# Kernel tuning notes

Measured on AMD Instinct MI355X. Metric: run time of the kernel, lower is better.

Reference implementation:

```python
import jax, jax.numpy as jnp
import numpy as np
from jax import lax

N_EXPERTS = 8
TOP_K_EXPERTS = 2
N_PRIMITIVES = 16
TOP_K_PRIM = 4
RANK = 64
D_MODEL = 512
D_FF = 2048
BATCH, SEQ = 8, 2048
TEMPERATURE = 1.0
EPS = 1e-8


def setup_inputs() -> dict:
    key = jax.random.key(0)
    ks = jax.random.split(key, 8)
    x = jax.random.normal(ks[0], (BATCH, SEQ, D_MODEL), dtype=jnp.float32)
    Wr = jax.random.normal(ks[1], (N_EXPERTS, D_MODEL), dtype=jnp.float32) * 0.02
    fc1_logits = jax.random.normal(ks[2], (N_EXPERTS, N_PRIMITIVES), dtype=jnp.float32)
    fc2_logits = jax.random.normal(ks[3], (N_EXPERTS, N_PRIMITIVES), dtype=jnp.float32)
    A1 = jax.random.normal(ks[4], (N_PRIMITIVES, D_MODEL, RANK), dtype=jnp.float32) * 0.02
    B1 = jax.random.normal(ks[5], (N_PRIMITIVES, RANK, D_FF), dtype=jnp.float32) * 0.02
    A2 = jax.random.normal(ks[6], (N_PRIMITIVES, D_FF, RANK), dtype=jnp.float32) * 0.02
    B2 = jax.random.normal(ks[7], (N_PRIMITIVES, RANK, D_MODEL), dtype=jnp.float32) * 0.02
    return {"x": x, "Wr": Wr, "fc1_logits": fc1_logits, "fc2_logits": fc2_logits,
            "A1": A1, "B1": B1, "A2": A2, "B2": B2}


def _compose_fused(logits, A, B):
    """Build per-expert fused low-rank maps from primitive bank.
    logits: (E, P); A: (P, d_in, r); B: (P, r, d_out).
    Returns A_cat (E, d_in, k*r), B_cat (E, k*r, d_out)."""
    w = jax.nn.softmax(logits / TEMPERATURE, axis=-1)            # (E, P)
    top_w, top_idx = lax.top_k(w, TOP_K_PRIM)                     # (E, k)
    top_w = top_w / (top_w.sum(axis=-1, keepdims=True) + EPS)
    sqrt_w = jnp.sqrt(top_w + EPS)                                # (E, k)
    A_sel = A[top_idx] * sqrt_w[:, :, None, None]                 # (E, k, d_in, r)
    B_sel = B[top_idx] * sqrt_w[:, :, None, None]                 # (E, k, r, d_out)
    E = logits.shape[0]
    A_cat = jnp.transpose(A_sel, (0, 2, 1, 3)).reshape(E, A.shape[1], TOP_K_PRIM * RANK)
    B_cat = B_sel.reshape(E, TOP_K_PRIM * RANK, B.shape[2])
    return A_cat, B_cat


def reference(x, Wr, fc1_logits, fc2_logits, A1, B1, A2, B2):
    Bsz, S, D = x.shape
    T = Bsz * S
    xt = x.reshape(T, D)

    # --- router: top-k expert selection ---
    router_logits = xt @ Wr.T                                     # (T, E)
    router_probs = jax.nn.softmax(router_logits, axis=-1)         # (T, E)
    top_w, top_idx = lax.top_k(router_probs, TOP_K_EXPERTS)       # (T, K)
    top_w = top_w / (top_w.sum(axis=-1, keepdims=True) + EPS)
    rows = jnp.arange(T)[:, None]
    gate = jnp.zeros((T, N_EXPERTS), x.dtype).at[rows, top_idx].add(top_w)
    expert_mask = jnp.zeros((T, N_EXPERTS), x.dtype).at[rows, top_idx].set(1.0)

    # --- load balancing aux loss (Switch Transformer) ---
    tokens_per_expert = expert_mask.sum(axis=0)
    f = tokens_per_expert / (tokens_per_expert.sum() + EPS)
    P = router_probs.mean(axis=0)
    aux_loss = N_EXPERTS * jnp.sum(f * P)

    # --- per-expert composed FFN over shared primitive banks ---
    A1c, B1c = _compose_fused(fc1_logits, A1, B1)                 # (E, D, kr), (E, kr, Dff)
    A2c, B2c = _compose_fused(fc2_logits, A2, B2)                 # (E, Dff, kr), (E, kr, D)

    out = jnp.zeros((T, D), x.dtype)
    for e in range(N_EXPERTS):  # small fixed expert loop keeps peak memory at one expert's d_ff activation
        h = jax.nn.gelu((xt @ A1c[e]) @ B1c[e], approximate=False)  # (T, Dff)
        y = (h @ A2c[e]) @ B2c[e]                                   # (T, D)
        out = out + gate[:, e:e + 1] * y

    return out.reshape(Bsz, S, D), aux_loss
```

## Files before the change

kernel.cpp:

```cpp
#include <hip/hip_runtime.h>

#define T_TOK 16384
#define DM    512
#define DFF   2048
#define NE    8
#define NP    16
#define KP    4
#define RANK  64
#define KR    256
#define EPSF  1e-8f
#define CAP   6144
#define MT_E  48

typedef unsigned short u16;
typedef __bf16 bf16x8 __attribute__((ext_vector_type(8)));
typedef float  f32x4  __attribute__((ext_vector_type(4)));
typedef unsigned short u16x8v __attribute__((ext_vector_type(8)));
typedef unsigned short u16x4v __attribute__((ext_vector_type(4)));

typedef __attribute__((address_space(3))) void as3_void;
typedef __attribute__((address_space(1))) void as1_void;

__device__ __forceinline__ u16 f2bf(float f) {
  return __builtin_bit_cast(u16, (__bf16)f);
}
__device__ __forceinline__ float bf2f(u16 v) {
  unsigned int u = ((unsigned int)v) << 16;
  return __builtin_bit_cast(float, u);
}

__device__ __forceinline__ void gl_lds16(const u16* g, u16* l) {
  __builtin_amdgcn_global_load_lds((as1_void*)g, (as3_void*)l, 16, 0, 0);
}


__device__ __forceinline__ void stage_tile(const u16* g, int ld, u16* lds_tile, int tid) {
  int row = tid >> 3, cc = tid & 7;
#pragma unroll
  for (int ri = 0; ri < 4; ri++) {
    int rg = ri * 32 + row;
    gl_lds16(g + (size_t)rg * ld + ((cc ^ (rg & 7)) * 8), &lds_tile[rg * 64 + cc * 8]);
  }
}

__device__ __forceinline__ void mfma_block(const u16* As, const u16* Bs, f32x4 acc[4][4],
                                           int wm, int wn, int ln, int quad) {
  int sw = (ln & 7) << 3;
#pragma unroll
  for (int ks = 0; ks < 2; ks++) {
    bf16x8 af[4], bf[4];
    int co = (ks * 32 + quad * 8) ^ sw;
#pragma unroll
    for (int mt = 0; mt < 4; mt++)
      af[mt] = *(const bf16x8*)&As[(wm * 64 + mt * 16 + ln) * 64 + co];
#pragma unroll
    for (int nt = 0; nt < 4; nt++)
      bf[nt] = *(const bf16x8*)&Bs[(wn * 64 + nt * 16 + ln) * 64 + co];
    __builtin_amdgcn_s_setprio(1);
#pragma unroll
    for (int mt = 0; mt < 4; mt++)
#pragma unroll
      for (int nt = 0; nt < 4; nt++)
        acc[mt][nt] = __builtin_amdgcn_mfma_f32_16x16x32_bf16(af[mt], bf[nt], acc[mt][nt], 0, 0, 0);
    __builtin_amdgcn_s_setprio(0);
  }
}

__global__ void zero_kernel(int* __restrict__ cnt, float* __restrict__ probsum) {
  int i = blockIdx.x * 256 + threadIdx.x;
  if (i < NE) cnt[i] = 0;
  if (i >= NE && i < NE + NE * 64) probsum[i - NE] = 0.f;
}

__global__ void compose_meta(const float* __restrict__ fc1, const float* __restrict__ fc2,
                             float* __restrict__ sw1, int* __restrict__ idx1,
                             float* __restrict__ sw2, int* __restrict__ idx2) {
  int tid = threadIdx.x;
  if (tid >= 16) return;
  const float* src = (tid < 8) ? fc1 : fc2;
  float* sw = (tid < 8) ? sw1 : sw2;
  int*  idx = (tid < 8) ? idx1 : idx2;
  int e = tid & 7;
  float wv[NP];
  float mx = -1e30f;
  for (int p = 0; p < NP; p++) { wv[p] = src[e * NP + p]; mx = fmaxf(mx, wv[p]); }
  float sum = 0.f;
  for (int p = 0; p < NP; p++) { wv[p] = __expf(wv[p] - mx); sum += wv[p]; }
  float inv = 1.f / sum;
  for (int p = 0; p < NP; p++) wv[p] *= inv;
  float tw[KP]; int ti[KP];
  for (int k = 0; k < KP; k++) {
    int best = 0; float bv = -1.f;
    for (int p = 0; p < NP; p++) if (wv[p] > bv) { bv = wv[p]; best = p; }
    tw[k] = bv; ti[k] = best; wv[best] = -2.f;
  }
  float ts = tw[0] + tw[1] + tw[2] + tw[3];
  float invt = 1.f / (ts + EPSF);
  for (int k = 0; k < KP; k++) {
    sw[e * KP + k] = sqrtf(tw[k] * invt + EPSF);
    idx[e * KP + k] = ti[k];
  }
}

__global__ __launch_bounds__(256) void build_AT(
    const float* __restrict__ A, const int* __restrict__ idx,
    const float* __restrict__ sw, u16* __restrict__ W, int D) {
  __shared__ u16 T[64 * 68];
  int ntile = D >> 6;
  int dt = blockIdx.x % ntile;
  int g  = blockIdx.x / ntile;
  int p = idx[g]; float s = sw[g];
  int d0 = dt * 64;
  int tid = threadIdx.x;
  {
    int rr = (tid & 15) * 4, dd = tid >> 4;
#pragma unroll
    for (int pass = 0; pass < 4; pass++) {
      int d = pass * 16 + dd;
      float4 v = *(const float4*)(A + ((size_t)p * D + d0 + d) * 64 + rr);
      T[(rr + 0) * 68 + d] = f2bf(v.x * s);
      T[(rr + 1) * 68 + d] = f2bf(v.y * s);
      T[(rr + 2) * 68 + d] = f2bf(v.z * s);
      T[(rr + 3) * 68 + d] = f2bf(v.w * s);
    }
  }
  __syncthreads();
  int e = g >> 2, k = g & 3;
  int c = (tid & 15) * 4, r = tid >> 4;
#pragma unroll
  for (int pass = 0; pass < 4; pass++) {
    int rr = pass * 16 + r;
    u16x4v o;
#pragma unroll
    for (int j = 0; j < 4; j++) o[j] = T[rr * 68 + c + j];
    *(u16x4v*)&W[((size_t)e * KR + k * 64 + rr) * D + d0 + c] = o;
  }
}

__global__ __launch_bounds__(256) void build_V1p(
    const float* __restrict__ B1, const int* __restrict__ idx1,
    const float* __restrict__ sw1, u16* __restrict__ V1p) {
  __shared__ u16 Tb[64 * 132];
  int bid = blockIdx.x;
  int p = bid & 3, f0i = (bid >> 2) & 15, e = bid >> 6;
  int prim = idx1[e * 4 + p];
  float s = sw1[e * 4 + p];
  int f0 = f0i * 128;
  int tid = threadIdx.x;
  {
    int r = tid >> 2, fq = (tid & 3) * 32;
#pragma unroll
    for (int q = 0; q < 8; q++) {
      int fl = fq + q * 4;
      float4 v = *(const float4*)(B1 + ((size_t)prim * RANK + r) * DFF + f0 + fl);
      u16x4v o;
      o[0] = f2bf(v.x * s); o[1] = f2bf(v.y * s);
      o[2] = f2bf(v.z * s); o[3] = f2bf(v.w * s);
      *(u16x4v*)&Tb[r * 132 + fl] = o;
    }
  }
  __syncthreads();
  u16* dst = V1p + ((size_t)e << 19) + f0i * 32768 + p * 8192;
#pragma unroll
  for (int it = 0; it < 4; it++) {
    int slot = it * 256 + tid;
    int lane = slot & 63, nt = (slot >> 6) & 1, ks = (slot >> 7) & 1, wv = slot >> 8;
    int ln = lane & 15, quad = lane >> 4;
    int fl = wv * 32 + nt * 16 + ln;
    int r0 = ks * 32 + quad * 8;
    u16x8v o;
#pragma unroll
    for (int j = 0; j < 8; j++) o[j] = Tb[(r0 + j) * 132 + fl];
    *(u16x8v*)&dst[(((wv * 2 + ks) * 2 + nt) * 64 + lane) * 8] = o;
  }
}

__global__ __launch_bounds__(256) void build_W2p(
    const float* __restrict__ A2, const int* __restrict__ idx2,
    const float* __restrict__ sw2, u16* __restrict__ W2p) {
  __shared__ u16 Ta[2 * 64 * 68];
  int bid = blockIdx.x;
  int c2 = bid & 3, f0i = (bid >> 2) & 15, e = bid >> 6;
  int hh = c2 >> 1, fi = c2 & 1;
  int f0 = f0i * 128 + fi * 64;
  int tid = threadIdx.x;
  {
    int kk = tid >> 7, row = (tid >> 1) & 63, half = tid & 1;
    int prim = idx2[e * 4 + hh * 2 + kk];
    float s = sw2[e * 4 + hh * 2 + kk];
#pragma unroll
    for (int q = 0; q < 8; q++) {
      int r = half * 32 + q * 4;
      float4 v = *(const float4*)(A2 + ((size_t)prim * DFF + f0 + row) * RANK + r);
      u16x4v o;
      o[0] = f2bf(v.x * s); o[1] = f2bf(v.y * s);
      o[2] = f2bf(v.z * s); o[3] = f2bf(v.w * s);
      *(u16x4v*)&Ta[(kk * 64 + row) * 68 + r] = o;
    }
  }
  __syncthreads();
  u16* dst = W2p + ((size_t)e << 19) + f0i * 32768 + c2 * 8192;
#pragma unroll
  for (int it = 0; it < 4; it++) {
    int slot = it * 256 + tid;
    int lane = slot & 63, nt = (slot >> 6) & 1, ks = (slot >> 7) & 1, wv = slot >> 8;
    int ln = lane & 15, quad = lane >> 4;
    int kk = wv >> 1;
    int r = (wv & 1) * 32 + nt * 16 + ln;
    int fb = ks * 32 + quad * 8;
    u16x8v o;
#pragma unroll
    for (int j = 0; j < 8; j++) o[j] = Ta[(kk * 64 + fb + j) * 68 + r];
    *(u16x8v*)&dst[(((wv * 2 + ks) * 2 + nt) * 64 + lane) * 8] = o;
  }
}

__global__ void build_V2(const float* __restrict__ B2,
                         const float* __restrict__ sw2, const int* __restrict__ idx2,
                         u16* __restrict__ V2) {
  const int S4 = NE * DM * KR;
  int j = blockIdx.x * 256 + threadIdx.x;
  if (j < S4) {
    int kr = j & 255; int d = (j >> 8) & 511; int e = j >> 17;
    int k = kr >> 6, r = kr & 63; int p = idx2[e * 4 + k];
    V2[j] = f2bf(B2[((size_t)p * RANK + r) * DM + d] * sw2[e * 4 + k]);
  }
}

__global__ __launch_bounds__(256) void router_kernel(
    const float* __restrict__ x, const float* __restrict__ Wr,
    float* __restrict__ probsum, int* __restrict__ eidx,
    float* __restrict__ gate) {
  __shared__ float wr_s[NE * 4 * 132];
  __shared__ float ps_s[NE];
  int tid = threadIdx.x;
  if (tid < NE) ps_s[tid] = 0.f;
  for (int i = tid; i < NE * DM; i += 256) {
    int e = i >> 9, k = i & 511;
    wr_s[(e * 4 + (k >> 7)) * 132 + (k & 127)] = Wr[i];
  }
  __syncthreads();
  int lane = tid & 63, wv = tid >> 6;
  int tl = lane & 15, sl = lane >> 4;
  int t = blockIdx.x * 64 + wv * 16 + tl;
  const float* xp = x + (size_t)t * DM + sl * 128;
  const float* wp = &wr_s[sl * 132];
  float acc[NE];
#pragma unroll
  for (int e = 0; e < NE; e++) acc[e] = 0.f;
  for (int c = 0; c < 32; c++) {
    float4 xv = *(const float4*)(xp + c * 4);
#pragma unroll
    for (int e = 0; e < NE; e++) {
      float4 w4 = *(const float4*)(wp + e * 4 * 132 + c * 4);
      acc[e] += xv.x * w4.x + xv.y * w4.y + xv.z * w4.z + xv.w * w4.w;
    }
  }
#pragma unroll
  for (int e = 0; e < NE; e++) {
    acc[e] += __shfl_xor(acc[e], 16, 64);
    acc[e] += __shfl_xor(acc[e], 32, 64);
  }
  if (sl == 0) {
    float mx = acc[0];
#pragma unroll
    for (int e = 1; e < NE; e++) mx = fmaxf(mx, acc[e]);
    float pe[NE]; float sum = 0.f;
#pragma unroll
    for (int e = 0; e < NE; e++) { pe[e] = __expf(acc[e] - mx); sum += pe[e]; }
    float inv = 1.f / sum;
#pragma unroll
    for (int e = 0; e < NE; e++) pe[e] *= inv;
    int i0 = 0;
#pragma unroll
    for (int e = 1; e < NE; e++) if (pe[e] > pe[i0]) i0 = e;
    int i1 = (i0 == 0) ? 1 : 0;
#pragma unroll
    for (int e = 0; e < NE; e++) if (e != i0 && pe[e] > pe[i1]) i1 = e;
    float p0 = pe[i0], p1 = pe[i1];
    float gd = 1.f / (p0 + p1 + EPSF);
    eidx[t] = i0 | (i1 << 3);
    gate[i0 * T_TOK + t] = p0 * gd;
    gate[i1 * T_TOK + t] = p1 * gd;
#pragma unroll
    for (int e = 0; e < NE; e++) atomicAdd(&ps_s[e], pe[e]);
  }
  __syncthreads();
  if (tid < NE) atomicAdd(&probsum[tid * 64 + (blockIdx.x & 63)], ps_s[tid]);
}

__global__ void scatter_kernel(const int* __restrict__ eidx,
                               int* __restrict__ cnt, int* __restrict__ perm,
                               int* __restrict__ slots) {
  __shared__ int hist[NE], base[NE];
  int tid = threadIdx.x;
  if (tid < NE) hist[tid] = 0;
  __syncthreads();
  int t = blockIdx.x * 256 + tid;
  int pk = eidx[t];
  int e0 = pk & 7, e1 = (pk >> 3) & 7;
  int p0 = atomicAdd(&hist[e0], 1);
  int p1 = atomicAdd(&hist[e1], 1);
  __syncthreads();
  if (tid < NE) base[tid] = atomicAdd(&cnt[tid], hist[tid]);
  __syncthreads();
  int g0 = base[e0] + p0; if (g0 >= CAP) g0 = CAP - 1;
  int g1 = base[e1] + p1; if (g1 >= CAP) g1 = CAP - 1;
  perm[e0 * T_TOK + g0] = t;
  perm[e1 * T_TOK + g1] = t;
  slots[t * 2]     = e0 * CAP + g0;
  slots[t * 2 + 1] = e1 * CAP + g1;
}

__global__ void aux_kernel(const int* __restrict__ cnt, const float* __restrict__ probsum,
                           float* __restrict__ aux_out) {
  int lane = threadIdx.x;
  if (lane >= 64) return;
  float s[NE];
#pragma unroll
  for (int e = 0; e < NE; e++) {
    float v = probsum[e * 64 + lane];
#pragma unroll
    for (int off = 32; off > 0; off >>= 1) v += __shfl_xor(v, off, 64);
    s[e] = v;
  }
  if (lane == 0) {
    float c[NE]; float cs = 0.f;
    for (int e = 0; e < NE; e++) { c[e] = (float)cnt[e]; cs += c[e]; }
    float aux = 0.f;
    for (int e = 0; e < NE; e++)
      aux += (c[e] / (cs + EPSF)) * (s[e] / (float)T_TOK);
    *aux_out = (float)NE * aux;
  }
}


__global__ __launch_bounds__(256) void k1_u(
    const float* __restrict__ x, const int* __restrict__ cnt,
    const int* __restrict__ perm, const u16* __restrict__ W1,
    u16* __restrict__ u) {
  __shared__ __align__(16) u16 As[8192], Bs[8192];
  __shared__ int tok_s[128];
  int bid = blockIdx.x;
  int e = bid & 7;
  int r0 = bid >> 3;
  int ntile = r0 & 1, mt = r0 >> 1;
  int m0 = mt << 7;
  int cntE = cnt[e];
  if (m0 >= cntE) return;
  int tid = threadIdx.x;
  if (tid < 128) {
    int mm = m0 + tid; if (mm > cntE - 1) mm = cntE - 1;
    tok_s[tid] = perm[e * T_TOK + mm];
  }
  __syncthreads();
  const u16* Bbase = W1 + (size_t)e * KR * DM + (size_t)(ntile * 128) * DM;
  int wv = tid >> 6, lane = tid & 63;
  int wm = wv >> 1, wn = wv & 1, ln = lane & 15, quad = lane >> 4;
  f32x4 acc[4][4];
#pragma unroll
  for (int a = 0; a < 4; a++)
#pragma unroll
    for (int b = 0; b < 4; b++) acc[a][b] = (f32x4){0.f, 0.f, 0.f, 0.f};
  for (int k0 = 0; k0 < DM; k0 += 64) {
    for (int i = tid; i < 2048; i += 256) {
      int row = i >> 4, c4 = i & 15;
      float4 v = *(const float4*)(x + (size_t)tok_s[row] * DM + k0 + c4 * 4);
      u16x4v o; o[0] = f2bf(v.x); o[1] = f2bf(v.y); o[2] = f2bf(v.z); o[3] = f2bf(v.w);
      *(u16x4v*)&As[row * 64 + ((c4 * 4) ^ ((row & 7) << 3))] = o;
    }
    stage_tile(Bbase + k0, DM, Bs, tid);
    __syncthreads();
    mfma_block(As, Bs, acc, wm, wn, ln, quad);
    __syncthreads();
  }
  int slot0 = e * CAP + m0;
#pragma unroll
  for (int mt2 = 0; mt2 < 4; mt2++)
#pragma unroll
    for (int nt = 0; nt < 4; nt++)
#pragma unroll
      for (int r = 0; r < 4; r++) {
        int row = wm * 64 + mt2 * 16 + quad * 4 + r;
        int col = ntile * 128 + wn * 64 + nt * 16 + ln;
        u[(size_t)(slot0 + row) * KR + col] = f2bf(acc[mt2][nt][r]);
      }
}

__global__ __launch_bounds__(256, 2) void k23(
    const u16* __restrict__ u, const int* __restrict__ cnt,
    const u16* __restrict__ V1p, const u16* __restrict__ W2p,
    u16* __restrict__ t) {
  __shared__ __align__(16) u16 Us[64 * 256];
  __shared__ __align__(16) u16 Hs[64 * 128];
  int bid = blockIdx.x;
  int e = bid & 7, mt = bid >> 3;
  int m0 = mt << 6;
  int cntE = cnt[e];
  if (m0 >= cntE) return;
  int tid = threadIdx.x;
  int slot0 = e * CAP + m0;
  const u16* ub = u + (size_t)slot0 * KR;

#pragma unroll
  for (int r = 0; r < 8; r++) {
    int i = r * 256 + tid;
    int row = i >> 5, cc = i & 31;
    gl_lds16(ub + (size_t)row * 256 + ((cc ^ (row & 7)) * 8), &Us[i * 8]);
  }
  __syncthreads();

  int wv = tid >> 6, lane = tid & 63;
  int ln = lane & 15, quad = lane >> 4;
  int sw = (ln & 7) << 3;
  const u16* V1w = V1p + ((size_t)e << 19) + wv * 2048 + lane * 8;
  const u16* W2w = W2p + ((size_t)e << 19) + wv * 2048 + lane * 8;

  f32x4 tacc[4][4];
#pragma unroll
  for (int a = 0; a < 4; a++)
#pragma unroll
    for (int b = 0; b < 4; b++) tacc[a][b] = (f32x4){0.f, 0.f, 0.f, 0.f};
  f32x4 hacc[4][2];

  for (int f0i = 0; f0i < 16; f0i++) {
    const u16* V1f = V1w + f0i * 32768;
    const u16* W2f = W2w + f0i * 32768;
#pragma unroll
    for (int p = 0; p < 4; p++) {
      bf16x8 bf[2][2], af[2][4];
#pragma unroll
      for (int ks = 0; ks < 2; ks++)
#pragma unroll
        for (int nt = 0; nt < 2; nt++)
          bf[ks][nt] = *(const bf16x8*)&V1f[p * 8192 + (ks * 2 + nt) * 512];
#pragma unroll
      for (int ks = 0; ks < 2; ks++) {
        int cu = (p * 64 + ks * 32 + quad * 8) ^ sw;
#pragma unroll
        for (int m = 0; m < 4; m++)
          af[ks][m] = *(const bf16x8*)&Us[(m * 16 + ln) * 256 + cu];
      }
      if (p == 0) {
#pragma unroll
        for (int a = 0; a < 4; a++)
#pragma unroll
          for (int b = 0; b < 2; b++) hacc[a][b] = (f32x4){0.f, 0.f, 0.f, 0.f};
      }
      __builtin_amdgcn_s_setprio(1);
#pragma unroll
      for (int ks = 0; ks < 2; ks++)
#pragma unroll
        for (int m = 0; m < 4; m++)
#pragma unroll
          for (int nt = 0; nt < 2; nt++)
            hacc[m][nt] = __builtin_amdgcn_mfma_f32_16x16x32_bf16(af[ks][m], bf[ks][nt], hacc[m][nt], 0, 0, 0);
      __builtin_amdgcn_s_setprio(0);
    }
    __syncthreads();
#pragma unroll
    for (int m = 0; m < 4; m++)
#pragma unroll
      for (int nt = 0; nt < 2; nt++)
#pragma unroll
        for (int r = 0; r < 4; r++) {
          int row = m * 16 + quad * 4 + r;
          int col = wv * 32 + nt * 16 + ln;
          float v = hacc[m][nt][r];
          float s = 1.f / (1.f + __expf(-1.702f * v));
          Hs[(row << 7) + (col ^ ((row & 7) << 3))] = f2bf(v * s);
        }
    __syncthreads();
#pragma unroll
    for (int c2 = 0; c2 < 4; c2++) {
      const int hh = c2 >> 1, fi = c2 & 1;
      bf16x8 bf[2][2], af[2][4];
#pragma unroll
      for (int ks = 0; ks < 2; ks++)
#pragma unroll
        for (int nt = 0; nt < 2; nt++)
          bf[ks][nt] = *(const bf16x8*)&W2f[c2 * 8192 + (ks * 2 + nt) * 512];
#pragma unroll
      for (int ks = 0; ks < 2; ks++) {
        int ch = (fi * 64 + ks * 32 + quad * 8) ^ sw;
#pragma unroll
        for (int m = 0; m < 4; m++)
          af[ks][m] = *(const bf16x8*)&Hs[((m * 16 + ln) << 7) + ch];
      }
      __builtin_amdgcn_s_setprio(1);
#pragma unroll
      for (int ks = 0; ks < 2; ks++)
#pragma unroll
        for (int m = 0; m < 4; m++)
#pragma unroll
          for (int nt = 0; nt < 2; nt++)
            tacc[m][hh * 2 + nt] = __builtin_amdgcn_mfma_f32_16x16x32_bf16(af[ks][m], bf[ks][nt], tacc[m][hh * 2 + nt], 0, 0, 0);
      __builtin_amdgcn_s_setprio(0);
    }
  }
#pragma unroll
  for (int m = 0; m < 4; m++)
#pragma unroll
    for (int hh = 0; hh < 2; hh++)
#pragma unroll
      for (int nt = 0; nt < 2; nt++)
#pragma unroll
        for (int r = 0; r < 4; r++) {
          int row = m * 16 + quad * 4 + r;
          int col = hh * 128 + wv * 32 + nt * 16 + ln;
          t[(size_t)(slot0 + row) * KR + col] = f2bf(tacc[m][hh * 2 + nt][r]);
        }
}

__global__ __launch_bounds__(256) void k4_y(
    const u16* __restrict__ t, const int* __restrict__ cnt,
    const int* __restrict__ perm, const float* __restrict__ gate,
    const u16* __restrict__ V2, u16* __restrict__ y) {
  __shared__ __align__(16) u16 As[8192], Bs[8192];
  __shared__ float g_s[128];
  int bid = blockIdx.x;
  int e = bid & 7;
  int r0 = bid >> 3;
  int ntile = r0 & 3, mt = r0 >> 2;
  int m0 = mt << 7;
  int cntE = cnt[e];
  if (m0 >= cntE) return;
  int tid = threadIdx.x;
  if (tid < 128) {
    int mm = m0 + tid; if (mm > cntE - 1) mm = cntE - 1;
    int tk = perm[e * T_TOK + mm];
    g_s[tid] = gate[e * T_TOK + tk];
  }
  __syncthreads();
  int slot0 = e * CAP + m0;
  const u16* Abase = t + (size_t)slot0 * KR;
  const u16* Bbase = V2 + (size_t)e * DM * KR + (size_t)(ntile * 128) * KR;
  int wv = tid >> 6, lane = tid & 63;
  int wm = wv >> 1, wn = wv & 1, ln = lane & 15, quad = lane >> 4;
  f32x4 acc[4][4];
#pragma unroll
  for (int a = 0; a < 4; a++)
#pragma unroll
    for (int b = 0; b < 4; b++) acc[a][b] = (f32x4){0.f, 0.f, 0.f, 0.f};
  for (int k0 = 0; k0 < KR; k0 += 64) {
    stage_tile(Abase + k0, KR, As, tid);
    stage_tile(Bbase + k0, KR, Bs, tid);
    __syncthreads();
    mfma_block(As, Bs, acc, wm, wn, ln, quad);
    __syncthreads();
  }
#pragma unroll
  for (int mt2 = 0; mt2 < 4; mt2++)
#pragma unroll
    for (int nt = 0; nt < 4; nt++)
#pragma unroll
      for (int r = 0; r < 4; r++) {
        int row = wm * 64 + mt2 * 16 + quad * 4 + r;
        int col = ntile * 128 + wn * 64 + nt * 16 + ln;
        y[(size_t)(slot0 + row) * DM + col] = f2bf(acc[mt2][nt][r] * g_s[row]);
      }
}

__global__ void gather_kernel(const u16* __restrict__ y, const int* __restrict__ slots,
                              float* __restrict__ out) {
  int idx = blockIdx.x * 256 + threadIdx.x;
  int t = idx >> 7, c4 = (idx & 127) * 4;
  int sA = slots[t * 2], sB = slots[t * 2 + 1];
  u16x4v a = *(const u16x4v*)&y[(size_t)sA * DM + c4];
  u16x4v b = *(const u16x4v*)&y[(size_t)sB * DM + c4];
  float4 o;
  o.x = bf2f(a[0]) + bf2f(b[0]);
  o.y = bf2f(a[1]) + bf2f(b[1]);
  o.z = bf2f(a[2]) + bf2f(b[2]);
  o.w = bf2f(a[3]) + bf2f(b[3]);
  *(float4*)&out[(size_t)t * DM + c4] = o;
}

extern "C" void kernel_launch(void* const* d_in, const int* in_sizes, int n_in,
                              void* d_out, int out_size, void* d_ws, size_t ws_size,
                              hipStream_t stream) {
  const float* x   = (const float*)d_in[0];
  const float* Wr  = (const float*)d_in[1];
  const float* fc1 = (const float*)d_in[2];
  const float* fc2 = (const float*)d_in[3];
  const float* A1  = (const float*)d_in[4];
  const float* B1  = (const float*)d_in[5];
  const float* A2  = (const float*)d_in[6];
  const float* B2  = (const float*)d_in[7];
  float* out = (float*)d_out;

  char* ws = (char*)d_ws;
  float* sw1     = (float*)(ws + 0);
  int*   idx1    = (int*)(ws + 512);
  float* sw2     = (float*)(ws + 1024);
  int*   idx2    = (int*)(ws + 1536);
  int*   cnt     = (int*)(ws + 2048);
  float* probsum = (float*)(ws + 2560);
  int*   eidx    = (int*)(ws + 8192);
  int*   slots   = (int*)(ws + 8192 + 65536);
  float* gate    = (float*)(ws + 8192 + 65536 + 131072);
  int*   perm    = (int*)(ws + 8192 + 65536 + 131072 + 524288);
  u16*   W1      = (u16*)(ws + 8192 + 65536 + 131072 + 2 * 524288);
  u16*   V1p     = W1 + 1048576;
  u16*   W2p     = V1p + 4194304;
  u16*   V2      = W2p + 4194304;
  char*  endW    = (char*)(V2 + 1048576);
  u16*   u_buf   = (u16*)endW;
  u16*   t_buf   = (u16*)(endW + 25165824);
  u16*   y_buf   = (u16*)(endW + 2 * 25165824);

  zero_kernel<<<3, 256, 0, stream>>>(cnt, probsum);
  compose_meta<<<1, 64, 0, stream>>>(fc1, fc2, sw1, idx1, sw2, idx2);
  build_AT<<<32 * (DM / 64), 256, 0, stream>>>(A1, idx1, sw1, W1, DM);
  build_V1p<<<512, 256, 0, stream>>>(B1, idx1, sw1, V1p);
  build_W2p<<<512, 256, 0, stream>>>(A2, idx2, sw2, W2p);
  build_V2<<<4096, 256, 0, stream>>>(B2, sw2, idx2, V2);
  router_kernel<<<T_TOK / 64, 256, 0, stream>>>(x, Wr, probsum, eidx, gate);
  scatter_kernel<<<T_TOK / 256, 256, 0, stream>>>(eidx, cnt, perm, slots);
  aux_kernel<<<1, 64, 0, stream>>>(cnt, probsum, out + (out_size - 1));

  k1_u<<<2 * NE * MT_E, 256, 0, stream>>>(x, cnt, perm, W1, u_buf);
  k23<<<NE * (CAP / 64), 256, 0, stream>>>(u_buf, cnt, V1p, W2p, t_buf);
  k4_y<<<4 * NE * MT_E, 256, 0, stream>>>(t_buf, cnt, perm, gate, V2, y_buf);
  gather_kernel<<<T_TOK * DM / 4 / 256, 256, 0, stream>>>(y_buf, slots, out);
}
```

Measured before the change: 360.1 us.

## Pre-pack W1 and V2 into MFMA fragment layout and load B operands directly

Replaces build_AT and build_V2 with kernels that write the composed W1 and V2 weights in a per-lane MFMA fragment order. k1_u and k4_y then read their B fragments straight from global memory into registers instead of staging a B tile through LDS, which halves their shared memory use. The new build_V2p also uses tiled LDS transposes instead of a strided element-wise gather. The aim is less LDS traffic, lower LDS footprint for occupancy and a cheaper V2 build. The risk is exposed global-load latency on B fragments, since they are not double-buffered.

```diff
diff --git a/kernel.cpp b/kernel.cpp
--- a/kernel.cpp
+++ b/kernel.cpp
@@ -40,29 +40,6 @@
   for (int ri = 0; ri < 4; ri++) {
     int rg = ri * 32 + row;
     gl_lds16(g + (size_t)rg * ld + ((cc ^ (rg & 7)) * 8), &lds_tile[rg * 64 + cc * 8]);
-  }
-}
-
-__device__ __forceinline__ void mfma_block(const u16* As, const u16* Bs, f32x4 acc[4][4],
-                                           int wm, int wn, int ln, int quad) {
-  int sw = (ln & 7) << 3;
-#pragma unroll
-  for (int ks = 0; ks < 2; ks++) {
-    bf16x8 af[4], bf[4];
-    int co = (ks * 32 + quad * 8) ^ sw;
-#pragma unroll
-    for (int mt = 0; mt < 4; mt++)
-      af[mt] = *(const bf16x8*)&As[(wm * 64 + mt * 16 + ln) * 64 + co];
-#pragma unroll
-    for (int nt = 0; nt < 4; nt++)
-      bf[nt] = *(const bf16x8*)&Bs[(wn * 64 + nt * 16 + ln) * 64 + co];
-    __builtin_amdgcn_s_setprio(1);
-#pragma unroll
-    for (int mt = 0; mt < 4; mt++)
-#pragma unroll
-      for (int nt = 0; nt < 4; nt++)
-        acc[mt][nt] = __builtin_amdgcn_mfma_f32_16x16x32_bf16(af[mt], bf[nt], acc[mt][nt], 0, 0, 0);
-    __builtin_amdgcn_s_setprio(0);
   }
 }
 
@@ -102,38 +79,42 @@
   }
 }
 
-__global__ __launch_bounds__(256) void build_AT(
-    const float* __restrict__ A, const int* __restrict__ idx,
-    const float* __restrict__ sw, u16* __restrict__ W, int D) {
-  __shared__ u16 T[64 * 68];
-  int ntile = D >> 6;
-  int dt = blockIdx.x % ntile;
-  int g  = blockIdx.x / ntile;
-  int p = idx[g]; float s = sw[g];
-  int d0 = dt * 64;
+__global__ __launch_bounds__(256) void build_W1p(
+    const float* __restrict__ A1, const int* __restrict__ idx1,
+    const float* __restrict__ sw1, u16* __restrict__ W1p) {
+  __shared__ u16 Ta[2 * 64 * 68];
+  int bid = blockIdx.x;
+  int k0i = bid & 7, ntile = (bid >> 3) & 1, e = bid >> 4;
+  int d0 = k0i * 64;
   int tid = threadIdx.x;
   {
-    int rr = (tid & 15) * 4, dd = tid >> 4;
-#pragma unroll
-    for (int pass = 0; pass < 4; pass++) {
-      int d = pass * 16 + dd;
-      float4 v = *(const float4*)(A + ((size_t)p * D + d0 + d) * 64 + rr);
-      T[(rr + 0) * 68 + d] = f2bf(v.x * s);
-      T[(rr + 1) * 68 + d] = f2bf(v.y * s);
-      T[(rr + 2) * 68 + d] = f2bf(v.z * s);
-      T[(rr + 3) * 68 + d] = f2bf(v.w * s);
-    }
-  }
-  __syncthreads();
-  int e = g >> 2, k = g & 3;
-  int c = (tid & 15) * 4, r = tid >> 4;
-#pragma unroll
-  for (int pass = 0; pass < 4; pass++) {
-    int rr = pass * 16 + r;
-    u16x4v o;
-#pragma unroll
-    for (int j = 0; j < 4; j++) o[j] = T[rr * 68 + c + j];
-    *(u16x4v*)&W[((size_t)e * KR + k * 64 + rr) * D + d0 + c] = o;
+    int kk = tid >> 7, row = (tid >> 1) & 63, half = tid & 1;
+    int prim = idx1[e * 4 + ntile * 2 + kk];
+    float s = sw1[e * 4 + ntile * 2 + kk];
+#pragma unroll
+    for (int q = 0; q < 8; q++) {
+      int r = half * 32 + q * 4;
+      float4 v = *(const float4*)(A1 + ((size_t)prim * DM + d0 + row) * RANK + r);
+      u16x4v o;
+      o[0] = f2bf(v.x * s); o[1] = f2bf(v.y * s);
+      o[2] = f2bf(v.z * s); o[3] = f2bf(v.w * s);
+      *(u16x4v*)&Ta[(kk * 64 + row) * 68 + r] = o;
+    }
+  }
+  __syncthreads();
+  u16* dst = W1p + ((size_t)(e * 2 + ntile) * 8 + k0i) * 8192;
+#pragma unroll
+  for (int it = 0; it < 4; it++) {
+    int slot = it * 256 + tid;
+    int lane = slot & 63, rest = slot >> 6;
+    int nt = rest & 3, ks = (rest >> 2) & 1, wn = rest >> 3;
+    int ln = lane & 15, quad = lane >> 4;
+    int r = nt * 16 + ln;
+    int db = ks * 32 + quad * 8;
+    u16x8v o;
+#pragma unroll
+    for (int j = 0; j < 8; j++) o[j] = Ta[(wn * 64 + db + j) * 68 + r];
+    *(u16x8v*)&dst[((wn * 8 + ks * 4 + nt) * 64 + lane) * 8] = o;
   }
 }
 
@@ -215,15 +196,41 @@
   }
 }
 
-__global__ void build_V2(const float* __restrict__ B2,
-                         const float* __restrict__ sw2, const int* __restrict__ idx2,
-                         u16* __restrict__ V2) {
-  const int S4 = NE * DM * KR;
-  int j = blockIdx.x * 256 + threadIdx.x;
-  if (j < S4) {
-    int kr = j & 255; int d = (j >> 8) & 511; int e = j >> 17;
-    int k = kr >> 6, r = kr & 63; int p = idx2[e * 4 + k];
-    V2[j] = f2bf(B2[((size_t)p * RANK + r) * DM + d] * sw2[e * 4 + k]);
+__global__ __launch_bounds__(256) void build_V2p(
+    const float* __restrict__ B2, const int* __restrict__ idx2,
+    const float* __restrict__ sw2, u16* __restrict__ V2p) {
+  __shared__ u16 Tb[64 * 132];
+  int bid = blockIdx.x;
+  int k0i = bid & 3, ntile = (bid >> 2) & 3, e = bid >> 4;
+  int prim = idx2[e * 4 + k0i];
+  float s = sw2[e * 4 + k0i];
+  int tid = threadIdx.x;
+  {
+    int r = tid >> 2, dq = (tid & 3) * 32;
+#pragma unroll
+    for (int q = 0; q < 8; q++) {
+      int dd = dq + q * 4;
+      float4 v = *(const float4*)(B2 + ((size_t)prim * RANK + r) * DM + ntile * 128 + dd);
+      u16x4v o;
+      o[0] = f2bf(v.x * s); o[1] = f2bf(v.y * s);
+      o[2] = f2bf(v.z * s); o[3] = f2bf(v.w * s);
+      *(u16x4v*)&Tb[r * 132 + dd] = o;
+    }
+  }
+  __syncthreads();
+  u16* dst = V2p + ((size_t)(e * 4 + ntile) * 4 + k0i) * 8192;
+#pragma unroll
+  for (int it = 0; it < 4; it++) {
+    int slot = it * 256 + tid;
+    int lane = slot & 63, rest = slot >> 6;
+    int nt = rest & 3, ks = (rest >> 2) & 1, wn = rest >> 3;
+    int ln = lane & 15, quad = lane >> 4;
+    int dd = wn * 64 + nt * 16 + ln;
+    int r0 = ks * 32 + quad * 8;
+    u16x8v o;
+#pragma unroll
+    for (int j = 0; j < 8; j++) o[j] = Tb[(r0 + j) * 132 + dd];
+    *(u16x8v*)&dst[((wn * 8 + ks * 4 + nt) * 64 + lane) * 8] = o;
   }
 }
 
@@ -337,9 +344,9 @@
 
 __global__ __launch_bounds__(256) void k1_u(
     const float* __restrict__ x, const int* __restrict__ cnt,
-    const int* __restrict__ perm, const u16* __restrict__ W1,
+    const int* __restrict__ perm, const u16* __restrict__ W1p,
     u16* __restrict__ u) {
-  __shared__ __align__(16) u16 As[8192], Bs[8192];
+  __shared__ __align__(16) u16 As[8192];
   __shared__ int tok_s[128];
   int bid = blockIdx.x;
   int e = bid & 7;
@@ -354,24 +361,45 @@
     tok_s[tid] = perm[e * T_TOK + mm];
   }
   __syncthreads();
-  const u16* Bbase = W1 + (size_t)e * KR * DM + (size_t)(ntile * 128) * DM;
   int wv = tid >> 6, lane = tid & 63;
   int wm = wv >> 1, wn = wv & 1, ln = lane & 15, quad = lane >> 4;
+  int sw = (ln & 7) << 3;
+  const u16* Wbase = W1p + ((size_t)(e * 2 + ntile) * 8) * 8192 + (wn * 8 * 64 + lane) * 8;
   f32x4 acc[4][4];
 #pragma unroll
   for (int a = 0; a < 4; a++)
 #pragma unroll
     for (int b = 0; b < 4; b++) acc[a][b] = (f32x4){0.f, 0.f, 0.f, 0.f};
-  for (int k0 = 0; k0 < DM; k0 += 64) {
+  for (int k0i = 0; k0i < 8; k0i++) {
+    bf16x8 bf[2][4];
+    const u16* Wf = Wbase + (size_t)k0i * 8192;
+#pragma unroll
+    for (int ks = 0; ks < 2; ks++)
+#pragma unroll
+      for (int nt = 0; nt < 4; nt++)
+        bf[ks][nt] = *(const bf16x8*)&Wf[(ks * 4 + nt) * 512];
     for (int i = tid; i < 2048; i += 256) {
       int row = i >> 4, c4 = i & 15;
-      float4 v = *(const float4*)(x + (size_t)tok_s[row] * DM + k0 + c4 * 4);
+      float4 v = *(const float4*)(x + (size_t)tok_s[row] * DM + k0i * 64 + c4 * 4);
       u16x4v o; o[0] = f2bf(v.x); o[1] = f2bf(v.y); o[2] = f2bf(v.z); o[3] = f2bf(v.w);
       *(u16x4v*)&As[row * 64 + ((c4 * 4) ^ ((row & 7) << 3))] = o;
     }
-    stage_tile(Bbase + k0, DM, Bs, tid);
     __syncthreads();
-    mfma_block(As, Bs, acc, wm, wn, ln, quad);
+#pragma unroll
+    for (int ks = 0; ks < 2; ks++) {
+      bf16x8 af[4];
+      int co = (ks * 32 + quad * 8) ^ sw;
+#pragma unroll
+      for (int mt2 = 0; mt2 < 4; mt2++)
+        af[mt2] = *(const bf16x8*)&As[(wm * 64 + mt2 * 16 + ln) * 64 + co];
+      __builtin_amdgcn_s_setprio(1);
+#pragma unroll
+      for (int mt2 = 0; mt2 < 4; mt2++)
+#pragma unroll
+        for (int nt = 0; nt < 4; nt++)
+          acc[mt2][nt] = __builtin_amdgcn_mfma_f32_16x16x32_bf16(af[mt2], bf[ks][nt], acc[mt2][nt], 0, 0, 0);
+      __builtin_amdgcn_s_setprio(0);
+    }
     __syncthreads();
   }
   int slot0 = e * CAP + m0;
@@ -515,8 +543,8 @@
 __global__ __launch_bounds__(256) void k4_y(
     const u16* __restrict__ t, const int* __restrict__ cnt,
     const int* __restrict__ perm, const float* __restrict__ gate,
-    const u16* __restrict__ V2, u16* __restrict__ y) {
-  __shared__ __align__(16) u16 As[8192], Bs[8192];
+    const u16* __restrict__ V2p, u16* __restrict__ y) {
+  __shared__ __align__(16) u16 As[8192];
   __shared__ float g_s[128];
   int bid = blockIdx.x;
   int e = bid & 7;
@@ -534,19 +562,40 @@
   __syncthreads();
   int slot0 = e * CAP + m0;
   const u16* Abase = t + (size_t)slot0 * KR;
-  const u16* Bbase = V2 + (size_t)e * DM * KR + (size_t)(ntile * 128) * KR;
   int wv = tid >> 6, lane = tid & 63;
   int wm = wv >> 1, wn = wv & 1, ln = lane & 15, quad = lane >> 4;
+  int sw = (ln & 7) << 3;
+  const u16* Wbase = V2p + ((size_t)(e * 4 + ntile) * 4) * 8192 + (wn * 8 * 64 + lane) * 8;
   f32x4 acc[4][4];
 #pragma unroll
   for (int a = 0; a < 4; a++)
 #pragma unroll
     for (int b = 0; b < 4; b++) acc[a][b] = (f32x4){0.f, 0.f, 0.f, 0.f};
-  for (int k0 = 0; k0 < KR; k0 += 64) {
-    stage_tile(Abase + k0, KR, As, tid);
-    stage_tile(Bbase + k0, KR, Bs, tid);
+  for (int k0i = 0; k0i < 4; k0i++) {
+    bf16x8 bf[2][4];
+    const u16* Wf = Wbase + (size_t)k0i * 8192;
+#pragma unroll
+    for (int ks = 0; ks < 2; ks++)
+#pragma unroll
+      for (int nt = 0; nt < 4; nt++)
+        bf[ks][nt] = *(const bf16x8*)&Wf[(ks * 4 + nt) * 512];
+    stage_tile(Abase + k0i * 64, KR, As, tid);
     __syncthreads();
-    mfma_block(As, Bs, acc, wm, wn, ln, quad);
+#pragma unroll
+    for (int ks = 0; ks < 2; ks++) {
+      bf16x8 af[4];
+      int co = (ks * 32 + quad * 8) ^ sw;
+#pragma unroll
+      for (int mt2 = 0; mt2 < 4; mt2++)
+        af[mt2] = *(const bf16x8*)&As[(wm * 64 + mt2 * 16 + ln) * 64 + co];
+      __builtin_amdgcn_s_setprio(1);
+#pragma unroll
+      for (int mt2 = 0; mt2 < 4; mt2++)
+#pragma unroll
+        for (int nt = 0; nt < 4; nt++)
+          acc[mt2][nt] = __builtin_amdgcn_mfma_f32_16x16x32_bf16(af[mt2], bf[ks][nt], acc[mt2][nt], 0, 0, 0);
+      __builtin_amdgcn_s_setprio(0);
+    }
     __syncthreads();
   }
 #pragma unroll
@@ -600,27 +649,27 @@
   int*   slots   = (int*)(ws + 8192 + 65536);
   float* gate    = (float*)(ws + 8192 + 65536 + 131072);
   int*   perm    = (int*)(ws + 8192 + 65536 + 131072 + 524288);
-  u16*   W1      = (u16*)(ws + 8192 + 65536 + 131072 + 2 * 524288);
-  u16*   V1p     = W1 + 1048576;
+  u16*   W1p     = (u16*)(ws + 8192 + 65536 + 131072 + 2 * 524288);
+  u16*   V1p     = W1p + 1048576;
   u16*   W2p     = V1p + 4194304;
-  u16*   V2      = W2p + 4194304;
-  char*  endW    = (char*)(V2 + 1048576);
+  u16*   V2p     = W2p + 4194304;
+  char*  endW    = (char*)(V2p + 1048576);
   u16*   u_buf   = (u16*)endW;
   u16*   t_buf   = (u16*)(endW + 25165824);
   u16*   y_buf   = (u16*)(endW + 2 * 25165824);
 
   zero_kernel<<<3, 256, 0, stream>>>(cnt, probsum);
   compose_meta<<<1, 64, 0, stream>>>(fc1, fc2, sw1, idx1, sw2, idx2);
-  build_AT<<<32 * (DM / 64), 256, 0, stream>>>(A1, idx1, sw1, W1, DM);
+  build_W1p<<<128, 256, 0, stream>>>(A1, idx1, sw1, W1p);
   build_V1p<<<512, 256, 0, stream>>>(B1, idx1, sw1, V1p);
   build_W2p<<<512, 256, 0, stream>>>(A2, idx2, sw2, W2p);
-  build_V2<<<4096, 256, 0, stream>>>(B2, sw2, idx2, V2);
+  build_V2p<<<128, 256, 0, stream>>>(B2, idx2, sw2, V2p);
   router_kernel<<<T_TOK / 64, 256, 0, stream>>>(x, Wr, probsum, eidx, gate);
   scatter_kernel<<<T_TOK / 256, 256, 0, stream>>>(eidx, cnt, perm, slots);
   aux_kernel<<<1, 64, 0, stream>>>(cnt, probsum, out + (out_size - 1));
 
-  k1_u<<<2 * NE * MT_E, 256, 0, stream>>>(x, cnt, perm, W1, u_buf);
+  k1_u<<<2 * NE * MT_E, 256, 0, stream>>>(x, cnt, perm, W1p, u_buf);
   k23<<<NE * (CAP / 64), 256, 0, stream>>>(u_buf, cnt, V1p, W2p, t_buf);
-  k4_y<<<4 * NE * MT_E, 256, 0, stream>>>(t_buf, cnt, perm, gate, V2, y_buf);
+  k4_y<<<4 * NE * MT_E, 256, 0, stream>>>(t_buf, cnt, perm, gate, V2p, y_buf);
   gather_kernel<<<T_TOK * DM / 4 / 256, 256, 0, stream>>>(y_buf, slots, out);
 }
```

After: 355.3 us. About the same (-1.3%).
